# Optimization experiments

Hardware: AMD Instinct MI355X
Metric: run time of the kernel (lower is better)

## Reference

```python
import jax, jax.numpy as jnp
from jax import lax
import numpy as np


def hac_round(X, W):
    """Avg-linkage HAC build+cut rounding of fractional SDP matrix X (D,D).
    Returns the 0/1 symmetric round_matrix with 1-diagonal."""
    D = X.shape[0]
    dt = X.dtype
    MAXD = jnp.max(jnp.abs(X)) * 1000.0  # _MAX_DIST sentinel
    max_sim = jnp.max(X)                 # max_similarity passed by forward()
    tril_mask = jnp.tril(jnp.ones((D, D), dtype=bool))
    # use_similarities=True branch: Y = MAXD*tril + (max_sim - X).triu(1)
    Y = jnp.where(tril_mask, MAXD, max_sim - X)
    values = jnp.min(Y, axis=1)
    indices = jnp.argmin(Y, axis=1)
    parents = jnp.arange(2 * D - 1)
    p2i = jnp.arange(2 * D - 1)   # parent_to_idx
    i2p = jnp.arange(D)           # idx_to_parent
    cs = jnp.ones(2 * D - 1, dtype=dt)
    energy = jnp.zeros(2 * D - 1, dtype=dt)
    clustering = jnp.zeros((2 * D - 1, D), dtype=dt)
    clustering = clustering.at[jnp.arange(D), jnp.arange(D)].set(jnp.arange(1, D + 1, dtype=dt))
    R = jnp.eye(D, dtype=dt)

    def body(i, st):
        Y, values, indices, parents, p2i, i2p, cs, energy, clustering, R = st
        max_node = D + i
        m1 = jnp.argmin(values)
        m2 = indices[m1]
        p1 = i2p[p2i[i2p[m1]]]
        p2 = i2p[p2i[i2p[m2]]]
        parents = parents.at[p1].set(max_node).at[p2].set(max_node)
        i2p = i2p.at[m1].set(max_node)
        p2i = p2i.at[max_node].set(m1)
        max_mask = Y == MAXD
        cs1, cs2 = cs[p1], cs[p2]
        ncs = cs1 + cs2
        cs = cs.at[max_node].set(ncs)
        # weighted average-linkage merged distances
        newv = (jnp.minimum(Y[m1, :], Y[:, m1]) * cs1 + jnp.minimum(Y[:, m2], Y[m2, :]) * cs2) / ncs
        Y = Y.at[:, m1].set(newv).at[m1, :].set(newv)
        Y = jnp.where(max_mask, MAXD, Y)
        Y = Y.at[:, m2].set(MAXD).at[m2, :].set(MAXD)
        values = values.at[m2].set(MAXD)
        vmask = values == MAXD
        values = jnp.where(vmask, MAXD, jnp.min(Y, axis=1))
        indices = jnp.argmin(Y, axis=1)
        # cut decision for the new internal node
        crow = clustering[p1] + clustering[p2]
        leaf = crow > 0                      # membership of new cluster
        lf = leaf.astype(dt)
        merge_e = lf @ (W @ lf)              # sum of W over leaf x leaf pairs
        e_sum = energy[p1] + energy[p2]
        take = merge_e >= e_sum
        energy = energy.at[max_node].set(jnp.where(take, merge_e, e_sum))
        crow = jnp.where(take & leaf, (max_node).astype(dt), crow)
        clustering = clustering.at[max_node].set(crow)
        R = jnp.where(take & (leaf[:, None] & leaf[None, :]), jnp.asarray(1.0, dt), R)
        return (Y, values, indices, parents, p2i, i2p, cs, energy, clustering, R)

    st = (Y, values, indices, parents, p2i, i2p, cs, energy, clustering, R)
    st = lax.fori_loop(0, D - 1, body, st)
    return st[-1]


def setup_inputs() -> dict:
    key = jax.random.key(0)
    k1, k2 = jax.random.split(key)
    D = 1024
    A = jax.random.uniform(k1, (D, D), dtype=jnp.float32)
    X = 0.5 * (A + A.T)                      # symmetric fractional decisions
    X = X.at[jnp.arange(D), jnp.arange(D)].set(1.0)  # 1-diagonal
    W = jnp.triu(jax.random.normal(k2, (D, D), dtype=jnp.float32), 1)  # triu(1) weights
    return {"X": X, "W": W}


def reference(X, W):
    # straight-through estimator: hard rounded solution, identity gradient w.r.t. X
    R = hac_round(X, W)
    return X + lax.stop_gradient(R - X)
```

## Files before the change

### kernel.cpp

```cpp
#include <hip/hip_runtime.h>
#include <stdint.h>

#define D 1024

typedef unsigned long long u64;
typedef unsigned int u32;

__device__ __forceinline__ u32 enc_f(float f) {
    u32 b = __float_as_uint(f);
    return (b & 0x80000000u) ? ~b : (b | 0x80000000u);
}
__device__ __forceinline__ float dec_f(u32 u) {
    u32 b = (u & 0x80000000u) ? (u ^ 0x80000000u) : ~u;
    return __uint_as_float(b);
}

__global__ void k_maxred(const float* __restrict__ X, u32* scal) {
    float mx = -INFINITY, ma = 0.f;
    int stride = gridDim.x * blockDim.x;
    for (int i = blockIdx.x * blockDim.x + threadIdx.x; i < D * D; i += stride) {
        float v = X[i];
        mx = fmaxf(mx, v);
        ma = fmaxf(ma, fabsf(v));
    }
    for (int o = 32; o; o >>= 1) {
        mx = fmaxf(mx, __shfl_xor(mx, o));
        ma = fmaxf(ma, __shfl_xor(ma, o));
    }
    if ((threadIdx.x & 63) == 0) {
        atomicMax(&scal[0], enc_f(mx));
        atomicMax(&scal[1], enc_f(ma));
    }
}

__global__ void k_init(const float* __restrict__ X, const float* __restrict__ W,
                       float* __restrict__ dist, float* __restrict__ cross,
                       const u32* __restrict__ scal) {
    int idx = blockIdx.x * blockDim.x + threadIdx.x;
    if (idx >= D * D) return;
    float max_sim = dec_f(scal[0]);
    float MAXD = __fmul_rn(dec_f(scal[1]), 1000.0f);
    int i = idx >> 10, j = idx & (D - 1);
    float x = X[idx];
    dist[idx] = (i == j) ? MAXD : __fsub_rn(max_sim, x);
    cross[idx] = (i == j) ? 0.0f : (W[idx] + W[j * D + i]);
}

__global__ void k_rowmin(const float* __restrict__ dist, float* __restrict__ values_g,
                         int* __restrict__ indices_g, const u32* __restrict__ scal) {
    int r = blockIdx.x;
    int lane = threadIdx.x;
    float MAXD = __fmul_rn(dec_f(scal[1]), 1000.0f);
    u64 best = ((u64)__float_as_uint(MAXD) << 32);
    const float* row = dist + (size_t)r * D;
    for (int j = lane; j < D; j += 64) {
        if (j > r) {
            u64 k = ((u64)__float_as_uint(row[j]) << 32) | (u32)j;
            if (k < best) best = k;
        }
    }
    for (int o = 32; o; o >>= 1) {
        u64 k2 = __shfl_xor(best, o);
        if (k2 < best) best = k2;
    }
    if (lane == 0) {
        values_g[r] = __uint_as_float((u32)(best >> 32));
        indices_g[r] = (int)(best & 0xffffffffu);
    }
}

__global__ void __launch_bounds__(1024) k_hac(
        float* __restrict__ dist, float* __restrict__ cross,
        const float* __restrict__ values_g, const int* __restrict__ indices_g,
        int* __restrict__ labels_g, const u32* __restrict__ scal) {
    __shared__ __align__(16) float values_l[D];
    __shared__ float values_stage[D];
    __shared__ int indices_l[D];
    __shared__ __align__(16) float newv_l[D];
    __shared__ float cs_l[D];
    __shared__ unsigned char dead_l[D];
    __shared__ unsigned char marked_l[D];
    __shared__ int slot_l[D];
    __shared__ int label_l[D];
    __shared__ double within_l[D];
    __shared__ double energy_l[D];
    __shared__ int rlist[2][D];
    __shared__ int nrec[2];
    __shared__ u64 s_best[2];
    __shared__ float s_cross12;
    __shared__ int s_takeP, s_m1P, s_labP;

    const int t = threadIdx.x;
    const int lane = t & 63, wid = t >> 6;
    const float MAXD = __fmul_rn(dec_f(scal[1]), 1000.0f);
    const u32 MAXDb = __float_as_uint(MAXD);

    values_l[t] = values_g[t];
    indices_l[t] = indices_g[t];
    cs_l[t] = 1.0f;
    dead_l[t] = 0;
    marked_l[t] = 0;
    slot_l[t] = t;
    label_l[t] = t;
    within_l[t] = 0.0;
    energy_l[t] = 0.0;
    if (t == 0) {
        s_takeP = 0; s_m1P = -1; s_labP = 0;
        nrec[0] = 0; nrec[1] = 0;
        s_best[0] = ~0ull; s_best[1] = ~0ull;
    }
    __syncthreads();
    {
        u64 key = ((u64)__float_as_uint(values_l[t]) << 32) | ((u32)t << 10) |
                  (u32)indices_l[t];
        for (int o = 32; o; o >>= 1) {
            u64 k2 = __shfl_xor(key, o);
            if (k2 < key) key = k2;
        }
        if (lane == 0) atomicMin(&s_best[0], key);
    }
    __syncthreads();

    for (int it = 0; it < D - 1; ++it) {
        const int cb = it & 1, pb = cb ^ 1;

        const u64 bk = s_best[cb];
        const int m1 = (int)((bk >> 10) & 1023);
        const int m2 = (int)(bk & 1023);
        const float cs1 = cs_l[m1], cs2 = cs_l[m2];
        const float ncs = __fadd_rn(cs1, cs2);
        const int pm1 = s_m1P;
        if (t == 0) s_best[pb] = ~0ull;

        if (marked_l[t]) { values_l[t] = values_stage[t]; marked_l[t] = 0; }
        if (t == m2) {
            dead_l[m2] = 1;
            values_l[m2] = MAXD;
            indices_l[m2] = 0;
        }
        const bool alive = !dead_l[t];

        float d1, d2, c1, c2;
        if (alive || t == m2) {
            d1 = dist[(size_t)m1 * D + t];
            d2 = dist[(size_t)m2 * D + t];
            c1 = cross[(size_t)m1 * D + t];
            c2 = cross[(size_t)m2 * D + t];
        }

        {
            int sl = slot_l[t];
            if (s_takeP && sl == pm1) label_l[t] = s_labP;
            if (sl == m2) slot_l[t] = m1;
        }

        float nv = MAXD, ncx = 0.0f;
        bool do_st = false;
        {
            if (t == m2) s_cross12 = c1;
            if (alive && t != m1) {
                nv = __fdiv_rn(__fadd_rn(__fmul_rn(d1, cs1), __fmul_rn(d2, cs2)), ncs);
                ncx = c1 + c2;
                dist[(size_t)m1 * D + t] = nv;
                cross[(size_t)m1 * D + t] = ncx;
                do_st = true;
            }
            newv_l[t] = nv;
        }
        {
            float v = values_l[t];
            if (t == m1) {
                values_l[t] = MAXD;
                marked_l[t] = 1;
            } else if (alive && v < MAXD) {
                int idx = indices_l[t];
                if (idx == m2) {
                    rlist[cb][atomicAdd(&nrec[cb], 1)] = t;
                    values_l[t] = MAXD;
                    marked_l[t] = 1;
                } else if (idx == m1) {
                    if (nv <= v) values_l[t] = nv;
                    else {
                        rlist[cb][atomicAdd(&nrec[cb], 1)] = t;
                        values_l[t] = MAXD;
                        marked_l[t] = 1;
                    }
                } else if (t < m1) {
                    if (nv < v) { values_l[t] = nv; indices_l[t] = m1; }
                    else if (nv == v && m1 < idx) indices_l[t] = m1;
                }
            }
        }
        __syncthreads();

        if (do_st) {
            dist[(size_t)t * D + m1] = nv;
            cross[(size_t)t * D + m1] = ncx;
        }
        if (t == m1) cs_l[m1] = ncs;
        const int n = nrec[cb];
        if (t == 0) nrec[pb] = 0;

        if (wid == 0) {
            if (lane == 0) {
                double merge_e = within_l[m1] + within_l[m2] + (double)s_cross12;
                double e_sum = energy_l[m1] + energy_l[m2];
                int take = (merge_e >= e_sum) ? 1 : 0;
                within_l[m1] = merge_e;
                energy_l[m1] = take ? merge_e : e_sum;
                s_takeP = take;
                s_m1P = m1;
                s_labP = D + it;
            }
            const float4* v4 = (const float4*)values_l;
            u64 bb = ~0ull;
#pragma unroll
            for (int c = 0; c < 4; ++c) {
                int fi = lane + 64 * c;
                float4 q = v4[fi];
                int b = fi << 2;
                u64 k;
                k = ((u64)__float_as_uint(q.x) << 32) | (u32)(b + 0); if (k < bb) bb = k;
                k = ((u64)__float_as_uint(q.y) << 32) | (u32)(b + 1); if (k < bb) bb = k;
                k = ((u64)__float_as_uint(q.z) << 32) | (u32)(b + 2); if (k < bb) bb = k;
                k = ((u64)__float_as_uint(q.w) << 32) | (u32)(b + 3); if (k < bb) bb = k;
            }
            for (int o = 32; o; o >>= 1) {
                u64 k2 = __shfl_xor(bb, o);
                if (k2 < bb) bb = k2;
            }
            if (lane == 0) {
                int r = (int)(bb & 1023);
                int idx = indices_l[r];
                atomicMin(&s_best[pb],
                          (bb & 0xffffffff00000000ull) | ((u32)r << 10) | (u32)idx);
            }
        } else if (wid == 1) {
            u64 bb = ((u64)MAXDb << 32);
            const float4* nv4 = (const float4*)newv_l;
            for (int c = lane; c < D / 4; c += 64) {
                float4 q = nv4[c];
                int j0 = c << 2;
#pragma unroll
                for (int e = 0; e < 4; ++e) {
                    int j = j0 + e;
                    float dv = (e == 0) ? q.x : (e == 1) ? q.y : (e == 2) ? q.z : q.w;
                    if (j > m1) {
                        u64 k = ((u64)__float_as_uint(dv) << 32) | (u32)j;
                        if (k < bb) bb = k;
                    }
                }
            }
            for (int o = 32; o; o >>= 1) {
                u64 k2 = __shfl_xor(bb, o);
                if (k2 < bb) bb = k2;
            }
            if (lane == 0) {
                values_stage[m1] = __uint_as_float((u32)(bb >> 32));
                indices_l[m1] = (int)(bb & 0xffffffffu);
                atomicMin(&s_best[pb],
                          (bb & 0xffffffff00000000ull) | ((u32)m1 << 10) | (bb & 1023));
            }
        } else {
            for (int q = wid - 2; q < n; q += 14) {
                const int r = rlist[cb][q];
                const float subst = newv_l[r];
                u64 bb = ((u64)MAXDb << 32);
                const float4* row4 = (const float4*)(dist + (size_t)r * D);
                for (int c = lane; c < D / 4; c += 64) {
                    float4 q4 = row4[c];
                    int j0 = c << 2;
#pragma unroll
                    for (int e = 0; e < 4; ++e) {
                        int j = j0 + e;
                        float dv = (e == 0) ? q4.x : (e == 1) ? q4.y : (e == 2) ? q4.z : q4.w;
                        if (j == m1) dv = subst;
                        if (j > r && !dead_l[j]) {
                            u64 k = ((u64)__float_as_uint(dv) << 32) | (u32)j;
                            if (k < bb) bb = k;
                        }
                    }
                }
                for (int o = 32; o; o >>= 1) {
                    u64 k2 = __shfl_xor(bb, o);
                    if (k2 < bb) bb = k2;
                }
                if (lane == 0) {
                    values_stage[r] = __uint_as_float((u32)(bb >> 32));
                    indices_l[r] = (int)(bb & 0xffffffffu);
                    atomicMin(&s_best[pb],
                              (bb & 0xffffffff00000000ull) | ((u32)r << 10) | (bb & 1023));
                }
            }
        }
        __syncthreads();
    }

    {
        int lab = label_l[t];
        if (s_takeP && slot_l[t] == s_m1P) lab = s_labP;
        labels_g[t] = lab;
    }
}

__global__ void k_out(const int* __restrict__ labels, float* __restrict__ out) {
    int idx = blockIdx.x * blockDim.x + threadIdx.x;
    if (idx >= D * D) return;
    int i = idx >> 10, j = idx & (D - 1);
    out[idx] = (i == j || labels[i] == labels[j]) ? 1.0f : 0.0f;
}

extern "C" void kernel_launch(void* const* d_in, const int* in_sizes, int n_in,
                              void* d_out, int out_size, void* d_ws, size_t ws_size,
                              hipStream_t stream) {
    const float* X = (const float*)d_in[0];
    const float* W = (const float*)d_in[1];

    char* ws = (char*)d_ws;
    const size_t MAT_BYTES = (size_t)D * D * sizeof(float);
    float* dist = (float*)ws;
    float* cross = (float*)(ws + MAT_BYTES);
    float* values_g = (float*)(ws + 2 * MAT_BYTES);
    int* indices_g = (int*)(ws + 2 * MAT_BYTES + 4096);
    int* labels_g = (int*)(ws + 2 * MAT_BYTES + 8192);
    u32* scal = (u32*)(ws + 2 * MAT_BYTES + 12288);

    hipMemsetAsync(scal, 0, 2 * sizeof(u32), stream);
    k_maxred<<<256, 256, 0, stream>>>(X, scal);
    k_init<<<(D * D) / 256, 256, 0, stream>>>(X, W, dist, cross, scal);
    k_rowmin<<<D, 64, 0, stream>>>(dist, values_g, indices_g, scal);
    k_hac<<<1, 1024, 0, stream>>>(dist, cross, values_g, indices_g, labels_g, scal);
    k_out<<<(D * D) / 256, 256, 0, stream>>>(labels_g, (float*)d_out);
}
```

Baseline: 3.498 ms.

## Interleave dist/cross into float2 and defer column stores past LDS-only barrier

Stores the distance and cross-weight matrices interleaved as float2 so each row/column access moves both values in a single load or store. The strided column write-back moves after the mid-iteration barrier and overlaps the row-min scans. The end-of-iteration barrier now waits only on LDS counters, not global memory. To keep this correct, the previous iteration's merged row is kept in shared history buffers and patched into the next iteration's reads, which adds subtle ordering risk if a global store is not yet visible. Row scans now read twice the bytes because of the interleave.

Measured after the change: 4.338 ms. +24.0%, slower.

```diff
diff --git a/kernel.cpp b/kernel.cpp
--- a/kernel.cpp
+++ b/kernel.cpp
@@ -13,6 +13,14 @@
 __device__ __forceinline__ float dec_f(u32 u) {
     u32 b = (u & 0x80000000u) ? (u ^ 0x80000000u) : ~u;
     return __uint_as_float(b);
+}
+
+__device__ __forceinline__ void barrier_lds_only() {
+    __builtin_amdgcn_sched_barrier(0);
+    asm volatile("s_waitcnt lgkmcnt(0)" ::: "memory");
+    __builtin_amdgcn_s_barrier();
+    asm volatile("" ::: "memory");
+    __builtin_amdgcn_sched_barrier(0);
 }
 
 __global__ void k_maxred(const float* __restrict__ X, u32* scal) {
@@ -34,28 +42,34 @@
 }
 
 __global__ void k_init(const float* __restrict__ X, const float* __restrict__ W,
-                       float* __restrict__ dist, float* __restrict__ cross,
-                       const u32* __restrict__ scal) {
+                       float2* __restrict__ dc, const u32* __restrict__ scal) {
     int idx = blockIdx.x * blockDim.x + threadIdx.x;
     if (idx >= D * D) return;
     float max_sim = dec_f(scal[0]);
     float MAXD = __fmul_rn(dec_f(scal[1]), 1000.0f);
     int i = idx >> 10, j = idx & (D - 1);
     float x = X[idx];
-    dist[idx] = (i == j) ? MAXD : __fsub_rn(max_sim, x);
-    cross[idx] = (i == j) ? 0.0f : (W[idx] + W[j * D + i]);
-}
-
-__global__ void k_rowmin(const float* __restrict__ dist, float* __restrict__ values_g,
+    float di = (i == j) ? MAXD : __fsub_rn(max_sim, x);
+    float cx = (i == j) ? 0.0f : (W[idx] + W[j * D + i]);
+    dc[idx] = make_float2(di, cx);
+}
+
+__global__ void k_rowmin(const float2* __restrict__ dc, float* __restrict__ values_g,
                          int* __restrict__ indices_g, const u32* __restrict__ scal) {
     int r = blockIdx.x;
     int lane = threadIdx.x;
     float MAXD = __fmul_rn(dec_f(scal[1]), 1000.0f);
     u64 best = ((u64)__float_as_uint(MAXD) << 32);
-    const float* row = dist + (size_t)r * D;
-    for (int j = lane; j < D; j += 64) {
-        if (j > r) {
-            u64 k = ((u64)__float_as_uint(row[j]) << 32) | (u32)j;
+    const float4* row4 = (const float4*)(dc + (size_t)r * D);
+    for (int c = lane; c < D / 2; c += 64) {
+        float4 q = row4[c];
+        int j0 = c << 1;
+        if (j0 > r) {
+            u64 k = ((u64)__float_as_uint(q.x) << 32) | (u32)j0;
+            if (k < best) best = k;
+        }
+        if (j0 + 1 > r) {
+            u64 k = ((u64)__float_as_uint(q.z) << 32) | (u32)(j0 + 1);
             if (k < best) best = k;
         }
     }
@@ -70,13 +84,14 @@
 }
 
 __global__ void __launch_bounds__(1024) k_hac(
-        float* __restrict__ dist, float* __restrict__ cross,
+        float2* __restrict__ dc,
         const float* __restrict__ values_g, const int* __restrict__ indices_g,
         int* __restrict__ labels_g, const u32* __restrict__ scal) {
     __shared__ __align__(16) float values_l[D];
     __shared__ float values_stage[D];
     __shared__ int indices_l[D];
-    __shared__ __align__(16) float newv_l[D];
+    __shared__ __align__(16) float newv_hist[2][D];
+    __shared__ __align__(16) float cross_hist[2][D];
     __shared__ float cs_l[D];
     __shared__ unsigned char dead_l[D];
     __shared__ unsigned char marked_l[D];
@@ -129,7 +144,8 @@
         const int m2 = (int)(bk & 1023);
         const float cs1 = cs_l[m1], cs2 = cs_l[m2];
         const float ncs = __fadd_rn(cs1, cs2);
-        const int pm1 = s_m1P;
+        const int p = s_m1P;
+        const int takeP = s_takeP, labP = s_labP;
         if (t == 0) s_best[pb] = ~0ull;
 
         if (marked_l[t]) { values_l[t] = values_stage[t]; marked_l[t] = 0; }
@@ -140,33 +156,39 @@
         }
         const bool alive = !dead_l[t];
 
-        float d1, d2, c1, c2;
+        float2 v1 = make_float2(0.f, 0.f), v2 = make_float2(0.f, 0.f);
         if (alive || t == m2) {
-            d1 = dist[(size_t)m1 * D + t];
-            d2 = dist[(size_t)m2 * D + t];
-            c1 = cross[(size_t)m1 * D + t];
-            c2 = cross[(size_t)m2 * D + t];
+            v1 = dc[(size_t)m1 * D + t];
+            v2 = dc[(size_t)m2 * D + t];
+        }
+        float d1 = v1.x, c1 = v1.y, d2 = v2.x, c2 = v2.y;
+        if (p >= 0) {
+            const float* nh_d = newv_hist[pb];
+            const float* nh_c = cross_hist[pb];
+            if (m1 == p)      { d1 = nh_d[t];  c1 = nh_c[t];  }
+            else if (t == p)  { d1 = nh_d[m1]; c1 = nh_c[m1]; }
+            if (m2 == p)      { d2 = nh_d[t];  c2 = nh_c[t];  }
+            else if (t == p)  { d2 = nh_d[m2]; c2 = nh_c[m2]; }
         }
 
         {
             int sl = slot_l[t];
-            if (s_takeP && sl == pm1) label_l[t] = s_labP;
+            if (takeP && sl == p) label_l[t] = labP;
             if (sl == m2) slot_l[t] = m1;
         }
 
         float nv = MAXD, ncx = 0.0f;
         bool do_st = false;
-        {
-            if (t == m2) s_cross12 = c1;
-            if (alive && t != m1) {
-                nv = __fdiv_rn(__fadd_rn(__fmul_rn(d1, cs1), __fmul_rn(d2, cs2)), ncs);
-                ncx = c1 + c2;
-                dist[(size_t)m1 * D + t] = nv;
-                cross[(size_t)m1 * D + t] = ncx;
-                do_st = true;
-            }
-            newv_l[t] = nv;
-        }
+        if (t == m2) s_cross12 = c1;
+        if (alive && t != m1) {
+            nv = __fdiv_rn(__fadd_rn(__fmul_rn(d1, cs1), __fmul_rn(d2, cs2)), ncs);
+            ncx = c1 + c2;
+            dc[(size_t)m1 * D + t] = make_float2(nv, ncx);
+            do_st = true;
+        }
+        newv_hist[cb][t] = nv;
+        cross_hist[cb][t] = ncx;
+
         {
             float v = values_l[t];
             if (t == m1) {
@@ -193,15 +215,12 @@
         }
         __syncthreads();
 
-        if (do_st) {
-            dist[(size_t)t * D + m1] = nv;
-            cross[(size_t)t * D + m1] = ncx;
-        }
         if (t == m1) cs_l[m1] = ncs;
         const int n = nrec[cb];
         if (t == 0) nrec[pb] = 0;
 
         if (wid == 0) {
+            if (do_st) dc[(size_t)t * D + m1] = make_float2(nv, ncx);
             if (lane == 0) {
                 double merge_e = within_l[m1] + within_l[m2] + (double)s_cross12;
                 double e_sum = energy_l[m1] + energy_l[m2];
@@ -236,8 +255,9 @@
                           (bb & 0xffffffff00000000ull) | ((u32)r << 10) | (u32)idx);
             }
         } else if (wid == 1) {
+            if (do_st) dc[(size_t)t * D + m1] = make_float2(nv, ncx);
             u64 bb = ((u64)MAXDb << 32);
-            const float4* nv4 = (const float4*)newv_l;
+            const float4* nv4 = (const float4*)newv_hist[cb];
             for (int c = lane; c < D / 4; c += 64) {
                 float4 q = nv4[c];
                 int j0 = c << 2;
@@ -264,21 +284,22 @@
         } else {
             for (int q = wid - 2; q < n; q += 14) {
                 const int r = rlist[cb][q];
-                const float subst = newv_l[r];
+                const float subst = newv_hist[cb][r];
                 u64 bb = ((u64)MAXDb << 32);
-                const float4* row4 = (const float4*)(dist + (size_t)r * D);
-                for (int c = lane; c < D / 4; c += 64) {
+                const float4* row4 = (const float4*)(dc + (size_t)r * D);
+                for (int c = lane; c < D / 2; c += 64) {
                     float4 q4 = row4[c];
-                    int j0 = c << 2;
-#pragma unroll
-                    for (int e = 0; e < 4; ++e) {
-                        int j = j0 + e;
-                        float dv = (e == 0) ? q4.x : (e == 1) ? q4.y : (e == 2) ? q4.z : q4.w;
-                        if (j == m1) dv = subst;
-                        if (j > r && !dead_l[j]) {
-                            u64 k = ((u64)__float_as_uint(dv) << 32) | (u32)j;
-                            if (k < bb) bb = k;
-                        }
+                    int j0 = c << 1;
+                    float dv0 = (j0 == m1) ? subst : q4.x;
+                    if (j0 > r && !dead_l[j0]) {
+                        u64 k = ((u64)__float_as_uint(dv0) << 32) | (u32)j0;
+                        if (k < bb) bb = k;
+                    }
+                    int j1 = j0 + 1;
+                    float dv1 = (j1 == m1) ? subst : q4.z;
+                    if (j1 > r && !dead_l[j1]) {
+                        u64 k = ((u64)__float_as_uint(dv1) << 32) | (u32)j1;
+                        if (k < bb) bb = k;
                     }
                 }
                 for (int o = 32; o; o >>= 1) {
@@ -292,8 +313,9 @@
                               (bb & 0xffffffff00000000ull) | ((u32)r << 10) | (bb & 1023));
                 }
             }
-        }
-        __syncthreads();
+            if (do_st) dc[(size_t)t * D + m1] = make_float2(nv, ncx);
+        }
+        barrier_lds_only();
     }
 
     {
@@ -318,8 +340,7 @@
 
     char* ws = (char*)d_ws;
     const size_t MAT_BYTES = (size_t)D * D * sizeof(float);
-    float* dist = (float*)ws;
-    float* cross = (float*)(ws + MAT_BYTES);
+    float2* dc = (float2*)ws;
     float* values_g = (float*)(ws + 2 * MAT_BYTES);
     int* indices_g = (int*)(ws + 2 * MAT_BYTES + 4096);
     int* labels_g = (int*)(ws + 2 * MAT_BYTES + 8192);
@@ -327,8 +348,8 @@
 
     hipMemsetAsync(scal, 0, 2 * sizeof(u32), stream);
     k_maxred<<<256, 256, 0, stream>>>(X, scal);
-    k_init<<<(D * D) / 256, 256, 0, stream>>>(X, W, dist, cross, scal);
-    k_rowmin<<<D, 64, 0, stream>>>(dist, values_g, indices_g, scal);
-    k_hac<<<1, 1024, 0, stream>>>(dist, cross, values_g, indices_g, labels_g, scal);
+    k_init<<<(D * D) / 256, 256, 0, stream>>>(X, W, dc, scal);
+    k_rowmin<<<D, 64, 0, stream>>>(dc, values_g, indices_g, scal);
+    k_hac<<<1, 1024, 0, stream>>>(dc, values_g, indices_g, labels_g, scal);
     k_out<<<(D * D) / 256, 256, 0, stream>>>(labels_g, (float*)d_out);
 }
```
